# Optimization experiments

Measured on AMD Instinct MI355X. Metric: run time of the kernel, lower is better.

Reference implementation:

```python
import jax, jax.numpy as jnp
import numpy as np

B, T, D = 4, 2048, 1024
H = 16
HD = D // H          # per-head dim (dk/heads = dv/heads = 64)
FF = 2048            # FFN default hidden_dim
EPS = 1e-5


def _ln(x, g, b):
    mu = jnp.mean(x, -1, keepdims=True)
    var = jnp.mean((x - mu) ** 2, -1, keepdims=True)
    return (x - mu) * jax.lax.rsqrt(var + EPS) * g + b


def setup_inputs() -> dict:
    key = jax.random.key(0)
    ks = jax.random.split(key, 12)
    s_in = 1.0 / np.sqrt(D)
    s_ff = 1.0 / np.sqrt(FF)
    return {
        "x": jax.random.normal(ks[0], (B, T, D), jnp.float32),
        # per-head projections stacked: [H, D, HD]
        "Wq": jax.random.uniform(ks[1], (H, D, HD), jnp.float32, -s_in, s_in),
        "bq": jnp.zeros((H, HD), jnp.float32),
        "Wk": jax.random.uniform(ks[2], (H, D, HD), jnp.float32, -s_in, s_in),
        "bk": jnp.zeros((H, HD), jnp.float32),
        "Wv": jax.random.uniform(ks[3], (H, D, HD), jnp.float32, -s_in, s_in),
        "bv": jnp.zeros((H, HD), jnp.float32),
        "Wo": jax.random.uniform(ks[4], (D, D), jnp.float32, -s_in, s_in),
        "bo": jnp.zeros((D,), jnp.float32),
        "ln1_g": jnp.ones((D,), jnp.float32),
        "ln1_b": jnp.zeros((D,), jnp.float32),
        "W1": jax.random.uniform(ks[5], (D, FF), jnp.float32, -s_in, s_in),
        "b1": jnp.zeros((FF,), jnp.float32),
        "W2": jax.random.uniform(ks[6], (FF, D), jnp.float32, -s_ff, s_ff),
        "b2": jnp.zeros((D,), jnp.float32),
        "ln2_g": jnp.ones((D,), jnp.float32),
        "ln2_b": jnp.zeros((D,), jnp.float32),
    }


def reference(x, Wq, bq, Wk, bk, Wv, bv, Wo, bo, ln1_g, ln1_b, W1, b1, W2, b2, ln2_g, ln2_b):
    # QKV projections (per-head Linear loop vectorized over H): [B,H,T,HD]
    q = jnp.einsum("btd,hdk->bhtk", x, Wq) + bq[:, None, :]
    k = jnp.einsum("btd,hdk->bhtk", x, Wk) + bk[:, None, :]
    v = jnp.einsum("btd,hdk->bhtk", x, Wv) + bv[:, None, :]
    # scaled dot-product attention; scale uses per-head dk = HD
    scores = jnp.einsum("bhtk,bhsk->bhts", q, k) / jnp.sqrt(jnp.float32(HD))
    weights = jax.nn.softmax(scores, axis=-1)
    ctx = jnp.einsum("bhts,bhsk->bhtk", weights, v)        # [B,H,T,HD]
    # concat heads along last dim (head order preserved) then output proj
    ctx = ctx.transpose(0, 2, 1, 3).reshape(B, T, D)
    c = ctx @ Wo + bo
    # residual + LayerNorm
    x = _ln(x + c, ln1_g, ln1_b)
    # FFN: Linear -> ReLU -> Linear
    y = jax.nn.relu(x @ W1 + b1) @ W2 + b2
    return _ln(x + y, ln2_g, ln2_b)
```

## Files before the change

kernel.cpp:

```cpp
#include <hip/hip_runtime.h>
#include <hip/hip_bf16.h>

#define BB 4
#define TT 2048
#define DD 1024
#define HH 16
#define HD 64
#define FF 2048
#define QSCL 0.1803368801111204f

typedef unsigned short u16;
typedef __bf16 bf16x8 __attribute__((ext_vector_type(8)));
typedef float f32x4 __attribute__((ext_vector_type(4)));
typedef float f32x16 __attribute__((ext_vector_type(16)));
typedef unsigned short u16x8 __attribute__((ext_vector_type(8)));
typedef unsigned short u16x4 __attribute__((ext_vector_type(4)));
typedef unsigned int u32x4 __attribute__((ext_vector_type(4)));

__device__ __forceinline__ u16 f2bf(float f) {
    return __builtin_bit_cast(u16, (__bf16)f);
}
__device__ __forceinline__ float bf2f(u16 u) {
    return __builtin_bit_cast(float, (unsigned)u << 16);
}
__device__ __forceinline__ float exp2fast(float x) {
    float r;
    asm("v_exp_f32 %0, %1" : "=v"(r) : "v"(x));
    return r;
}

__device__ __forceinline__ void gload16(const void* g, void* l) {
    __builtin_amdgcn_global_load_lds((const __attribute__((address_space(1))) void*)g,
                                     (__attribute__((address_space(3))) void*)l, 16, 0, 0);
}

__global__ __launch_bounds__(256) void convert_x(const float* __restrict__ in, u16* __restrict__ out, int n8) {
    int i = blockIdx.x * 256 + threadIdx.x;
    if (i >= n8) return;
    const float4* p = (const float4*)in + (size_t)i * 2;
    float4 a = p[0], b = p[1];
    u16x8 o;
    o[0] = f2bf(a.x); o[1] = f2bf(a.y); o[2] = f2bf(a.z); o[3] = f2bf(a.w);
    o[4] = f2bf(b.x); o[5] = f2bf(b.y); o[6] = f2bf(b.z); o[7] = f2bf(b.w);
    ((u16x8*)out)[i] = o;
}

__global__ __launch_bounds__(256) void transpose_conv(const float* __restrict__ in, u16* __restrict__ out, int R, int C) {
    __shared__ float tile[32][33];
    const int c0 = blockIdx.x * 32, r0 = blockIdx.y * 32;
    const int tx = threadIdx.x & 31, ty = threadIdx.x >> 5;
#pragma unroll
    for (int j = 0; j < 4; ++j) tile[ty + j * 8][tx] = in[(size_t)(r0 + ty + j * 8) * C + c0 + tx];
    __syncthreads();
#pragma unroll
    for (int j = 0; j < 4; ++j) out[(size_t)(c0 + ty + j * 8) * R + r0 + tx] = f2bf(tile[tx][ty + j * 8]);
}

__global__ __launch_bounds__(256) void qkv_transpose(const float* __restrict__ Wq, const float* __restrict__ Wk,
                                                     const float* __restrict__ Wv, u16* __restrict__ out) {
    __shared__ float tile[32][33];
    const int z = blockIdx.z, w = z >> 4, h = z & 15;
    const float* in = (w == 0 ? Wq : (w == 1 ? Wk : Wv)) + (size_t)h * (DD * HD);
    u16* op = out + (size_t)(w * 1024 + h * 64) * DD;
    const int c0 = blockIdx.x * 32, r0 = blockIdx.y * 32;
    const int tx = threadIdx.x & 31, ty = threadIdx.x >> 5;
#pragma unroll
    for (int j = 0; j < 4; ++j) tile[ty + j * 8][tx] = in[(size_t)(r0 + ty + j * 8) * HD + c0 + tx];
    __syncthreads();
#pragma unroll
    for (int j = 0; j < 4; ++j) op[(size_t)(c0 + ty + j * 8) * DD + r0 + tx] = f2bf(tile[tx][ty + j * 8]);
}

__global__ __launch_bounds__(256) void pack_bias(const float* __restrict__ bq, const float* __restrict__ bk,
                                                 const float* __restrict__ bv, float* __restrict__ out) {
    int i = blockIdx.x * 256 + threadIdx.x;
    if (i < 3072) {
        const float* s = i < 1024 ? bq : (i < 2048 ? bk : bv);
        out[i] = s[i & 1023];
    }
}

#define GBM 128
#define GBN 128
#define GBK 64

template <int EPI>
__global__ __launch_bounds__(256) void gemm_bt(const u16* __restrict__ A, const u16* __restrict__ Bt,
                                               const float* __restrict__ bias, const void* __restrict__ res,
                                               void* __restrict__ outp, void* __restrict__ outp2,
                                               int M, int N, int K) {
    __shared__ __align__(16) u16 sA[GBM * GBK];
    __shared__ __align__(16) u16 sB[GBN * GBK];
    const int t = threadIdx.x;
    const int lane = t & 63, wv = t >> 6;
    const int wm = (wv >> 1) * 64, wn = (wv & 1) * 64;
    const int lq = lane & 15, lk8 = (lane >> 4) * 8;
    const int nwg = gridDim.x * gridDim.y;
    const int bid = blockIdx.y * gridDim.x + blockIdx.x;
    const int swz = (bid & 7) * (nwg >> 3) + (bid >> 3);
    const int m0 = (swz / gridDim.x) * GBM, n0 = (swz % gridDim.x) * GBN;

    const int lr = lane >> 3, ch = lane & 7;
    const int colel = (ch ^ lr) << 3;
    const u16* Abase = A + (size_t)(m0 + wv * 32 + lr) * K + colel;
    const u16* Bbase = Bt + (size_t)(n0 + wv * 32 + lr) * K + colel;
    char* sAw = (char*)sA + wv * 32 * 128;
    char* sBw = (char*)sB + wv * 32 * 128;

    f32x4 acc[4][4];
#pragma unroll
    for (int i = 0; i < 4; ++i)
#pragma unroll
        for (int j = 0; j < 4; ++j) acc[i][j] = (f32x4){0.f, 0.f, 0.f, 0.f};

    for (int k0 = 0; k0 < K; k0 += GBK) {
#pragma unroll
        for (int i = 0; i < 4; ++i) {
            gload16(Abase + (size_t)i * 8 * K + k0, sAw + i * 1024);
            gload16(Bbase + (size_t)i * 8 * K + k0, sBw + i * 1024);
        }
        __syncthreads();
#pragma unroll
        for (int kk = 0; kk < 2; ++kk) {
            bf16x8 af[4], bfr[4];
#pragma unroll
            for (int mf = 0; mf < 4; ++mf) {
                int row = wm + mf * 16 + lq;
                int by = (row * 128 + kk * 64 + lk8 * 2) ^ ((row & 7) << 4);
                af[mf] = *(const bf16x8*)((const char*)sA + by);
            }
#pragma unroll
            for (int nf = 0; nf < 4; ++nf) {
                int row = wn + nf * 16 + lq;
                int by = (row * 128 + kk * 64 + lk8 * 2) ^ ((row & 7) << 4);
                bfr[nf] = *(const bf16x8*)((const char*)sB + by);
            }
#pragma unroll
            for (int mf = 0; mf < 4; ++mf)
#pragma unroll
                for (int nf = 0; nf < 4; ++nf)
                    acc[mf][nf] = __builtin_amdgcn_mfma_f32_16x16x32_bf16(af[mf], bfr[nf], acc[mf][nf], 0, 0, 0);
        }
        __syncthreads();
    }

    const int rbase = (lane >> 4) * 4;
#pragma unroll
    for (int mf = 0; mf < 4; ++mf) {
#pragma unroll
        for (int nf = 0; nf < 4; ++nf) {
            int gn = n0 + wn + nf * 16 + lq;
            float bv = bias[gn];
            if (EPI == 0) {
                int which = gn >> 10, hh = (gn >> 6) & 15, hd = gn & 63;
                int gm0 = m0 + wm + mf * 16 + rbase;
                int b = gm0 >> 11, tt2 = gm0 & 2047;
                if (which == 2) {
                    u16x4 pk;
#pragma unroll
                    for (int r = 0; r < 4; ++r) pk[r] = f2bf(acc[mf][nf][r] + bv);
                    *(u16x4*)((u16*)outp2 + ((size_t)(b * HH + hh) * HD + hd) * TT + tt2) = pk;
                } else {
                    float scl = (which == 0) ? QSCL : 1.f;
                    size_t off0 = (size_t)which * ((size_t)BB * HH * TT * HD) +
                                  ((size_t)(b * HH + hh) * TT + tt2) * HD + hd;
#pragma unroll
                    for (int r = 0; r < 4; ++r)
                        ((u16*)outp)[off0 + (size_t)r * HD] = f2bf((acc[mf][nf][r] + bv) * scl);
                }
            } else {
#pragma unroll
                for (int r = 0; r < 4; ++r) {
                    int gm = m0 + wm + mf * 16 + rbase + r;
                    size_t idx = (size_t)gm * N + gn;
                    float val = acc[mf][nf][r] + bv;
                    if (EPI == 2) {
                        ((u16*)outp)[idx] = f2bf(val > 0.f ? val : 0.f);
                    } else if (EPI == 1) {
                        ((u16*)outp)[idx] = f2bf(val + ((const float*)res)[idx]);
                    } else {
                        ((u16*)outp)[idx] = f2bf(val + bf2f(((const u16*)res)[idx]));
                    }
                }
            }
        }
    }
}

__global__ __launch_bounds__(512) void attn_kernel(const u16* __restrict__ qk, const u16* __restrict__ vt,
                                                   u16* __restrict__ ctx) {
    const int t = threadIdx.x, wv = t >> 6, lane = t & 63;
    const int l31 = lane & 31, hi = lane >> 5;
    const int lr = lane >> 3, ch = lane & 7;
    const int colel = (ch ^ lr) << 3;
    const int qt = blockIdx.x, bh = blockIdx.y;
    const size_t WSTR = (size_t)BB * HH * TT * HD;
    const u16* qp = qk + (size_t)bh * TT * HD;
    const u16* kp = qp + WSTR;
    const u16* vtp = vt + (size_t)bh * HD * TT;
    const int qr = qt * 256 + wv * 32;

    __shared__ __align__(16) u16 sK[2][64 * 64];
    __shared__ __align__(16) u16 sVt[2][64 * 64];

    const u16* kbase = kp + (size_t)(wv * 8 + lr) * HD + colel;
    const u16* vbase = vtp + (size_t)(wv * 8 + lr) * TT + colel;
    char* dK = (char*)sK + wv * 1024;
    char* dV = (char*)sVt + wv * 1024;

#define ATTN_STAGE(bufi, kb)                                        \
    do {                                                            \
        gload16(kbase + (size_t)(kb)*HD, dK + (bufi)*8192);         \
        gload16(vbase + (kb), dV + (bufi)*8192);                    \
    } while (0)

    bf16x8 qf[4];
#pragma unroll
    for (int c = 0; c < 4; ++c)
        qf[c] = *(const bf16x8*)(qp + (size_t)(qr + l31) * HD + c * 16 + 8 * hi);

    int off[2][4];
#pragma unroll
    for (int half = 0; half < 2; ++half)
#pragma unroll
        for (int c = 0; c < 4; ++c) {
            int row = half * 32 + l31;
            off[half][c] = row * 128 + (((c * 16 + 8 * hi) * 2) ^ ((row & 7) << 4));
        }

    f32x16 psv = (f32x16)0.f;
    f32x16 oacc[2];
    oacc[0] = (f32x16)0.f;
    oacc[1] = (f32x16)0.f;

    ATTN_STAGE(0, 0);

    const int NT = TT / 64;
    for (int kt = 0; kt < NT; ++kt) {
        const int cur = kt & 1;
        if (kt + 1 < NT) {
            ATTN_STAGE(cur ^ 1, (kt + 1) * 64);
            asm volatile("s_waitcnt vmcnt(2)" ::: "memory");
        } else {
            asm volatile("s_waitcnt vmcnt(0)" ::: "memory");
        }
        __builtin_amdgcn_s_barrier();
        __builtin_amdgcn_sched_barrier(0);

        const char* sKc = (const char*)sK + cur * 8192;
        const char* sVc = (const char*)sVt + cur * 8192;

        f32x16 sacc[2];
        sacc[0] = (f32x16)0.f;
        sacc[1] = (f32x16)0.f;
#pragma unroll
        for (int kb2 = 0; kb2 < 2; ++kb2)
#pragma unroll
            for (int c = 0; c < 4; ++c) {
                bf16x8 kf = *(const bf16x8*)(sKc + off[kb2][c]);
                sacc[kb2] = __builtin_amdgcn_mfma_f32_32x32x16_bf16(kf, qf[c], sacc[kb2], 0, 0, 0);
            }

#pragma unroll
        for (int kb2 = 0; kb2 < 2; ++kb2) {
#pragma unroll
            for (int i = 0; i < 16; ++i) sacc[kb2][i] = exp2fast(sacc[kb2][i]);
            psv += sacc[kb2];
        }

        bf16x8 pfrag[4];
#pragma unroll
        for (int kb2 = 0; kb2 < 2; ++kb2)
#pragma unroll
            for (int c2 = 0; c2 < 2; ++c2) {
                const int base = c2 * 8;
                unsigned a0, a1, b0, b1;
                asm("v_cvt_pk_bf16_f32 %0, %1, %2" : "=v"(a0) : "v"(sacc[kb2][base + 0]), "v"(sacc[kb2][base + 1]));
                asm("v_cvt_pk_bf16_f32 %0, %1, %2" : "=v"(a1) : "v"(sacc[kb2][base + 2]), "v"(sacc[kb2][base + 3]));
                asm("v_cvt_pk_bf16_f32 %0, %1, %2" : "=v"(b0) : "v"(sacc[kb2][base + 4]), "v"(sacc[kb2][base + 5]));
                asm("v_cvt_pk_bf16_f32 %0, %1, %2" : "=v"(b1) : "v"(sacc[kb2][base + 6]), "v"(sacc[kb2][base + 7]));
                asm("v_permlane32_swap_b32 %0, %1" : "+v"(a0), "+v"(b0));
                asm("v_permlane32_swap_b32 %0, %1" : "+v"(a1), "+v"(b1));
                u32x4 w = {a0, a1, b0, b1};
                pfrag[kb2 * 2 + c2] = __builtin_bit_cast(bf16x8, w);
            }

#pragma unroll
        for (int db = 0; db < 2; ++db)
#pragma unroll
            for (int kc = 0; kc < 4; ++kc) {
                bf16x8 vf = *(const bf16x8*)(sVc + off[db][kc]);
                oacc[db] = __builtin_amdgcn_mfma_f32_32x32x16_bf16(vf, pfrag[kc], oacc[db], 0, 0, 0);
            }

        __builtin_amdgcn_sched_barrier(0);
        __builtin_amdgcn_s_barrier();
    }

    float ls = 0.f;
#pragma unroll
    for (int i = 0; i < 16; ++i) ls += psv[i];
    ls += __shfl_xor(ls, 32);
    const float inv = 1.f / ls;

    const int b = bh >> 4, h = bh & 15;
    u16* orow = ctx + ((size_t)b * TT + (qr + l31)) * DD + h * HD;
#pragma unroll
    for (int db = 0; db < 2; ++db)
#pragma unroll
        for (int rq = 0; rq < 4; ++rq) {
            u16x4 ov;
#pragma unroll
            for (int j = 0; j < 4; ++j) ov[j] = f2bf(oacc[db][rq * 4 + j] * inv);
            *(u16x4*)(orow + db * 32 + rq * 8 + 4 * hi) = ov;
        }
#undef ATTN_STAGE
}

template <bool OUTF32>
__global__ __launch_bounds__(256) void ln_kernel(const u16* __restrict__ y, const float* __restrict__ g,
                                                 const float* __restrict__ b, float* __restrict__ of,
                                                 u16* __restrict__ ob) {
    const int row = blockIdx.x, t = threadIdx.x;
    const u16x4 raw = *(const u16x4*)(y + (size_t)row * DD + t * 4);
    float v0 = bf2f(raw[0]), v1 = bf2f(raw[1]), v2 = bf2f(raw[2]), v3 = bf2f(raw[3]);
    float s = v0 + v1 + v2 + v3;
    float q = v0 * v0 + v1 * v1 + v2 * v2 + v3 * v3;
#pragma unroll
    for (int m = 1; m < 64; m <<= 1) {
        s += __shfl_xor(s, m);
        q += __shfl_xor(q, m);
    }
    __shared__ float red[8];
    const int wv = t >> 6, ln = t & 63;
    if (ln == 0) {
        red[wv] = s;
        red[4 + wv] = q;
    }
    __syncthreads();
    s = red[0] + red[1] + red[2] + red[3];
    q = red[4] + red[5] + red[6] + red[7];
    const float mu = s * (1.f / DD);
    const float var = q * (1.f / DD) - mu * mu;
    const float rstd = rsqrtf(var + 1e-5f);
    const float4 gg = ((const float4*)g)[t];
    const float4 bb = ((const float4*)b)[t];
    float o0 = (v0 - mu) * rstd * gg.x + bb.x;
    float o1 = (v1 - mu) * rstd * gg.y + bb.y;
    float o2 = (v2 - mu) * rstd * gg.z + bb.z;
    float o3 = (v3 - mu) * rstd * gg.w + bb.w;
    if (OUTF32) {
        ((float4*)(of + (size_t)row * DD))[t] = (float4){o0, o1, o2, o3};
    } else {
        u16x4 u;
        u[0] = f2bf(o0); u[1] = f2bf(o1); u[2] = f2bf(o2); u[3] = f2bf(o3);
        *(u16x4*)(ob + (size_t)row * DD + t * 4) = u;
    }
}

extern "C" void kernel_launch(void* const* d_in, const int* in_sizes, int n_in,
                              void* d_out, int out_size, void* d_ws, size_t ws_size,
                              hipStream_t stream) {
    const float* x   = (const float*)d_in[0];
    const float* Wq  = (const float*)d_in[1];
    const float* bq  = (const float*)d_in[2];
    const float* Wk  = (const float*)d_in[3];
    const float* bk  = (const float*)d_in[4];
    const float* Wv  = (const float*)d_in[5];
    const float* bv  = (const float*)d_in[6];
    const float* Wo  = (const float*)d_in[7];
    const float* bo  = (const float*)d_in[8];
    const float* g1  = (const float*)d_in[9];
    const float* be1 = (const float*)d_in[10];
    const float* W1  = (const float*)d_in[11];
    const float* b1  = (const float*)d_in[12];
    const float* W2  = (const float*)d_in[13];
    const float* b2  = (const float*)d_in[14];
    const float* g2  = (const float*)d_in[15];
    const float* be2 = (const float*)d_in[16];
    float* out = (float*)d_out;

    char* ws = (char*)d_ws;
    u16*   xb    = (u16*)(ws + 0);
    u16*   wqkvt = (u16*)(ws + 16777216);
    u16*   wot   = (u16*)(ws + 23068672);
    u16*   w1t   = (u16*)(ws + 25165824);
    u16*   w2t   = (u16*)(ws + 29360128);
    float* bqkv  = (float*)(ws + 33554432);
    u16*   qkb   = (u16*)(ws + 33566720);
    u16*   vtb   = qkb + (size_t)2 * BB * HH * TT * HD;
    u16*   y1b   = (u16*)(ws + 83898368);
    u16*   x1b   = (u16*)(ws + 100675584);
    u16*   ctx   = xb;
    u16*   hbuf  = qkb;
    u16*   y2b   = y1b;

    const int M = BB * TT;

    convert_x<<<dim3((M * DD / 8 + 255) / 256), 256, 0, stream>>>(x, xb, M * DD / 8);
    qkv_transpose<<<dim3(2, 32, 48), 256, 0, stream>>>(Wq, Wk, Wv, wqkvt);
    transpose_conv<<<dim3(32, 32), 256, 0, stream>>>(Wo, wot, DD, DD);
    transpose_conv<<<dim3(64, 32), 256, 0, stream>>>(W1, w1t, DD, FF);
    transpose_conv<<<dim3(32, 64), 256, 0, stream>>>(W2, w2t, FF, DD);
    pack_bias<<<dim3(12), 256, 0, stream>>>(bq, bk, bv, bqkv);

    gemm_bt<0><<<dim3(3 * DD / GBN, M / GBM), 256, 0, stream>>>(xb, wqkvt, bqkv, nullptr, qkb, vtb, M, 3 * DD, DD);
    attn_kernel<<<dim3(TT / 256, BB * HH), 512, 0, stream>>>(qkb, vtb, ctx);
    gemm_bt<1><<<dim3(DD / GBN, M / GBM), 256, 0, stream>>>(ctx, wot, bo, x, y1b, nullptr, M, DD, DD);
    ln_kernel<false><<<dim3(M), 256, 0, stream>>>(y1b, g1, be1, nullptr, x1b);
    gemm_bt<2><<<dim3(FF / GBN, M / GBM), 256, 0, stream>>>(x1b, w1t, b1, nullptr, hbuf, nullptr, M, FF, DD);
    gemm_bt<3><<<dim3(DD / GBN, M / GBM), 256, 0, stream>>>(hbuf, w2t, b2, x1b, y2b, nullptr, M, DD, FF);
    ln_kernel<true><<<dim3(M), 256, 0, stream>>>(y2b, g2, be2, out, nullptr);
}
```

Baseline: 302.4 us.

## Add 256x256 ping-pong GEMM for QKV and FFN1, swizzle attention block order

Adds a new 512-thread GEMM kernel with 256x256 output tiles and a split-phase LDS pipeline. The pipeline interleaves async global-to-LDS loads with MFMA quarters, uses setprio and barriers between phases, and remaps workgroups for L2 locality. The QKV projection and first FFN GEMM now use it, and the attention grid is remapped so consecutive blocks share heads differently. The larger tiles are meant to raise arithmetic intensity and reduce global traffic, at the cost of high register pressure (128 accumulators per thread) and fewer workgroups.

```diff
diff --git a/kernel.cpp b/kernel.cpp
--- a/kernel.cpp
+++ b/kernel.cpp
@@ -28,7 +28,6 @@
     asm("v_exp_f32 %0, %1" : "=v"(r) : "v"(x));
     return r;
 }
-
 __device__ __forceinline__ void gload16(const void* g, void* l) {
     __builtin_amdgcn_global_load_lds((const __attribute__((address_space(1))) void*)g,
                                      (__attribute__((address_space(3))) void*)l, 16, 0, 0);
@@ -151,6 +150,181 @@
         for (int nf = 0; nf < 4; ++nf) {
             int gn = n0 + wn + nf * 16 + lq;
             float bv = bias[gn];
+#pragma unroll
+            for (int r = 0; r < 4; ++r) {
+                int gm = m0 + wm + mf * 16 + rbase + r;
+                size_t idx = (size_t)gm * N + gn;
+                float val = acc[mf][nf][r] + bv;
+                if (EPI == 2) {
+                    ((u16*)outp)[idx] = f2bf(val > 0.f ? val : 0.f);
+                } else if (EPI == 1) {
+                    ((u16*)outp)[idx] = f2bf(val + ((const float*)res)[idx]);
+                } else {
+                    ((u16*)outp)[idx] = f2bf(val + bf2f(((const u16*)res)[idx]));
+                }
+            }
+        }
+    }
+}
+
+template <int EPI>
+__global__ __launch_bounds__(512, 2) void gemm256(const u16* __restrict__ A, const u16* __restrict__ Bt,
+                                                  const float* __restrict__ bias,
+                                                  void* __restrict__ outp, void* __restrict__ outp2,
+                                                  int M, int N, int K) {
+    __shared__ __align__(16) u16 sA[256 * 64];
+    __shared__ __align__(16) u16 sB[256 * 64];
+    const int t = threadIdx.x;
+    const int lane = t & 63, wv = t >> 6;
+    const int wm = (wv >> 2) * 128, wn = (wv & 3) * 64;
+    const int lq = lane & 15, lk8 = (lane >> 4) * 8;
+    const int lr = lane >> 3, ch = lane & 7;
+    const int colel = (ch ^ lr) << 3;
+    const int nwg = gridDim.x * gridDim.y;
+    const int bid = blockIdx.y * gridDim.x + blockIdx.x;
+    const int swz = (bid & 7) * (nwg >> 3) + (bid >> 3);
+    const int m0 = (swz / gridDim.x) * 256, n0 = (swz % gridDim.x) * 256;
+
+    const u16* Ag = A + ((size_t)m0 + lr) * K + colel;
+    const u16* Bg = Bt + ((size_t)n0 + lr) * K + colel;
+
+#define STAGE_A(slot, k0)                                                          \
+    do {                                                                           \
+        _Pragma("unroll") for (int j = 0; j < 2; ++j) {                            \
+            int row0 = (slot)*64 + j * 128 + wv * 8;                               \
+            gload16(Ag + (size_t)row0 * K + (k0), (char*)sA + row0 * 128);         \
+        }                                                                          \
+    } while (0)
+#define STAGE_B(slot, k0)                                                          \
+    do {                                                                           \
+        _Pragma("unroll") for (int j = 0; j < 2; ++j) {                            \
+            int c = j * 8 + wv;                                                    \
+            int row0 = (c >> 2) * 64 + (slot)*32 + (c & 3) * 8;                    \
+            gload16(Bg + (size_t)row0 * K + (k0), (char*)sB + row0 * 128);         \
+        }                                                                          \
+    } while (0)
+
+    f32x4 acc[8][4];
+#pragma unroll
+    for (int i = 0; i < 8; ++i)
+#pragma unroll
+        for (int j = 0; j < 4; ++j) acc[i][j] = (f32x4){0.f, 0.f, 0.f, 0.f};
+
+    STAGE_A(0, 0);
+    STAGE_B(0, 0);
+    STAGE_B(1, 0);
+    STAGE_A(1, 0);
+    asm volatile("s_waitcnt vmcnt(4)" ::: "memory");
+    __builtin_amdgcn_s_barrier();
+
+    const int nk = K / 64;
+    for (int kt = 0; kt < nk; ++kt) {
+        const int k0 = kt * 64, k1 = k0 + 64;
+        const bool pf = (kt + 1 < nk);
+        bf16x8 a0[4][2], a1[4][2], b0[2][2], b1[2][2];
+
+#pragma unroll
+        for (int mf = 0; mf < 4; ++mf)
+#pragma unroll
+            for (int kk = 0; kk < 2; ++kk) {
+                int row = wm + mf * 16 + lq;
+                a0[mf][kk] = *(const bf16x8*)((const char*)sA + ((row * 128 + kk * 64 + lk8 * 2) ^ ((row & 7) << 4)));
+            }
+#pragma unroll
+        for (int nf = 0; nf < 2; ++nf)
+#pragma unroll
+            for (int kk = 0; kk < 2; ++kk) {
+                int row = wn + nf * 16 + lq;
+                b0[nf][kk] = *(const bf16x8*)((const char*)sB + ((row * 128 + kk * 64 + lk8 * 2) ^ ((row & 7) << 4)));
+            }
+        __builtin_amdgcn_s_barrier();
+        asm volatile("s_waitcnt lgkmcnt(0)" ::: "memory");
+        __builtin_amdgcn_sched_barrier(0);
+        __builtin_amdgcn_s_setprio(1);
+#pragma unroll
+        for (int mf = 0; mf < 4; ++mf)
+#pragma unroll
+            for (int nf = 0; nf < 2; ++nf) {
+                acc[mf][nf] = __builtin_amdgcn_mfma_f32_16x16x32_bf16(a0[mf][0], b0[nf][0], acc[mf][nf], 0, 0, 0);
+                acc[mf][nf] = __builtin_amdgcn_mfma_f32_16x16x32_bf16(a0[mf][1], b0[nf][1], acc[mf][nf], 0, 0, 0);
+            }
+        __builtin_amdgcn_s_setprio(0);
+        __builtin_amdgcn_sched_barrier(0);
+        asm volatile("s_waitcnt vmcnt(2)" ::: "memory");
+        __builtin_amdgcn_s_barrier();
+
+#pragma unroll
+        for (int nf = 0; nf < 2; ++nf)
+#pragma unroll
+            for (int kk = 0; kk < 2; ++kk) {
+                int row = wn + (nf + 2) * 16 + lq;
+                b1[nf][kk] = *(const bf16x8*)((const char*)sB + ((row * 128 + kk * 64 + lk8 * 2) ^ ((row & 7) << 4)));
+            }
+        if (pf) {
+            STAGE_A(0, k1);
+            STAGE_B(0, k1);
+        }
+        __builtin_amdgcn_s_barrier();
+        asm volatile("s_waitcnt lgkmcnt(0)" ::: "memory");
+        __builtin_amdgcn_sched_barrier(0);
+        __builtin_amdgcn_s_setprio(1);
+#pragma unroll
+        for (int mf = 0; mf < 4; ++mf)
+#pragma unroll
+            for (int nf = 0; nf < 2; ++nf) {
+                acc[mf][nf + 2] = __builtin_amdgcn_mfma_f32_16x16x32_bf16(a0[mf][0], b1[nf][0], acc[mf][nf + 2], 0, 0, 0);
+                acc[mf][nf + 2] = __builtin_amdgcn_mfma_f32_16x16x32_bf16(a0[mf][1], b1[nf][1], acc[mf][nf + 2], 0, 0, 0);
+            }
+        __builtin_amdgcn_s_setprio(0);
+        __builtin_amdgcn_sched_barrier(0);
+        asm volatile("s_waitcnt vmcnt(4)" ::: "memory");
+        __builtin_amdgcn_s_barrier();
+
+#pragma unroll
+        for (int mf = 0; mf < 4; ++mf)
+#pragma unroll
+            for (int kk = 0; kk < 2; ++kk) {
+                int row = wm + (mf + 4) * 16 + lq;
+                a1[mf][kk] = *(const bf16x8*)((const char*)sA + ((row * 128 + kk * 64 + lk8 * 2) ^ ((row & 7) << 4)));
+            }
+        if (pf) STAGE_B(1, k1);
+        __builtin_amdgcn_s_barrier();
+        asm volatile("s_waitcnt lgkmcnt(0)" ::: "memory");
+        __builtin_amdgcn_sched_barrier(0);
+        __builtin_amdgcn_s_setprio(1);
+#pragma unroll
+        for (int mf = 0; mf < 4; ++mf)
+#pragma unroll
+            for (int nf = 0; nf < 2; ++nf) {
+                acc[mf + 4][nf + 2] = __builtin_amdgcn_mfma_f32_16x16x32_bf16(a1[mf][0], b1[nf][0], acc[mf + 4][nf + 2], 0, 0, 0);
+                acc[mf + 4][nf + 2] = __builtin_amdgcn_mfma_f32_16x16x32_bf16(a1[mf][1], b1[nf][1], acc[mf + 4][nf + 2], 0, 0, 0);
+            }
+        __builtin_amdgcn_s_setprio(0);
+        __builtin_amdgcn_sched_barrier(0);
+        __builtin_amdgcn_s_barrier();
+
+        if (pf) STAGE_A(1, k1);
+        __builtin_amdgcn_s_setprio(1);
+#pragma unroll
+        for (int mf = 0; mf < 4; ++mf)
+#pragma unroll
+            for (int nf = 0; nf < 2; ++nf) {
+                acc[mf + 4][nf] = __builtin_amdgcn_mfma_f32_16x16x32_bf16(a1[mf][0], b0[nf][0], acc[mf + 4][nf], 0, 0, 0);
+                acc[mf + 4][nf] = __builtin_amdgcn_mfma_f32_16x16x32_bf16(a1[mf][1], b0[nf][1], acc[mf + 4][nf], 0, 0, 0);
+            }
+        __builtin_amdgcn_s_setprio(0);
+        __builtin_amdgcn_sched_barrier(0);
+        asm volatile("s_waitcnt vmcnt(4)" ::: "memory");
+        __builtin_amdgcn_s_barrier();
+    }
+
+    const int rbase = (lane >> 4) * 4;
+#pragma unroll
+    for (int mf = 0; mf < 8; ++mf) {
+#pragma unroll
+        for (int nf = 0; nf < 4; ++nf) {
+            int gn = n0 + wn + nf * 16 + lq;
+            float bv = bias[gn];
             if (EPI == 0) {
                 int which = gn >> 10, hh = (gn >> 6) & 15, hd = gn & 63;
                 int gm0 = m0 + wm + mf * 16 + rbase;
@@ -172,19 +346,14 @@
 #pragma unroll
                 for (int r = 0; r < 4; ++r) {
                     int gm = m0 + wm + mf * 16 + rbase + r;
-                    size_t idx = (size_t)gm * N + gn;
                     float val = acc[mf][nf][r] + bv;
-                    if (EPI == 2) {
-                        ((u16*)outp)[idx] = f2bf(val > 0.f ? val : 0.f);
-                    } else if (EPI == 1) {
-                        ((u16*)outp)[idx] = f2bf(val + ((const float*)res)[idx]);
-                    } else {
-                        ((u16*)outp)[idx] = f2bf(val + bf2f(((const u16*)res)[idx]));
-                    }
+                    ((u16*)outp)[(size_t)gm * N + gn] = f2bf(val > 0.f ? val : 0.f);
                 }
             }
         }
     }
+#undef STAGE_A
+#undef STAGE_B
 }
 
 __global__ __launch_bounds__(512) void attn_kernel(const u16* __restrict__ qk, const u16* __restrict__ vt,
@@ -193,7 +362,9 @@
     const int l31 = lane & 31, hi = lane >> 5;
     const int lr = lane >> 3, ch = lane & 7;
     const int colel = (ch ^ lr) << 3;
-    const int qt = blockIdx.x, bh = blockIdx.y;
+    const int bid = blockIdx.y * 8 + blockIdx.x;
+    const int swz = (bid & 7) * 64 + (bid >> 3);
+    const int qt = swz & 7, bh = swz >> 3;
     const size_t WSTR = (size_t)BB * HH * TT * HD;
     const u16* qp = qk + (size_t)bh * TT * HD;
     const u16* kp = qp + WSTR;
@@ -404,11 +575,11 @@
     transpose_conv<<<dim3(32, 64), 256, 0, stream>>>(W2, w2t, FF, DD);
     pack_bias<<<dim3(12), 256, 0, stream>>>(bq, bk, bv, bqkv);
 
-    gemm_bt<0><<<dim3(3 * DD / GBN, M / GBM), 256, 0, stream>>>(xb, wqkvt, bqkv, nullptr, qkb, vtb, M, 3 * DD, DD);
+    gemm256<0><<<dim3(3 * DD / 256, M / 256), 512, 0, stream>>>(xb, wqkvt, bqkv, qkb, vtb, M, 3 * DD, DD);
     attn_kernel<<<dim3(TT / 256, BB * HH), 512, 0, stream>>>(qkb, vtb, ctx);
     gemm_bt<1><<<dim3(DD / GBN, M / GBM), 256, 0, stream>>>(ctx, wot, bo, x, y1b, nullptr, M, DD, DD);
     ln_kernel<false><<<dim3(M), 256, 0, stream>>>(y1b, g1, be1, nullptr, x1b);
-    gemm_bt<2><<<dim3(FF / GBN, M / GBM), 256, 0, stream>>>(x1b, w1t, b1, nullptr, hbuf, nullptr, M, FF, DD);
+    gemm256<2><<<dim3(FF / 256, M / 256), 512, 0, stream>>>(x1b, w1t, b1, hbuf, nullptr, M, FF, DD);
     gemm_bt<3><<<dim3(DD / GBN, M / GBM), 256, 0, stream>>>(hbuf, w2t, b2, x1b, y2b, nullptr, M, DD, FF);
     ln_kernel<true><<<dim3(M), 256, 0, stream>>>(y2b, g2, be2, out, nullptr);
 }
```

Measured after the change: 299.3 us. No clear change (-1.0%).
